# Performance work log

Hardware: AMD Instinct MI355X
Metric: run time of the kernel (lower is better)

Reference implementation:

```python
import jax, jax.numpy as jnp
import numpy as np

IN_DIM = 1024
QK_DIM = 64
NHEADS = 12
HN_MULT = 4
BATCH = 2
SEQ = 2048
BETA = 1.0 / np.sqrt(QK_DIM)


def setup_inputs() -> dict:
    key = jax.random.key(0)
    kg, kq, kk, kw = jax.random.split(key, 4)
    scale = 1.0 / np.sqrt(IN_DIM)
    g = jax.random.normal(kg, (BATCH, SEQ, IN_DIM), dtype=jnp.float32)
    Wq = jax.random.normal(kq, (NHEADS, QK_DIM, IN_DIM), dtype=jnp.float32) * scale
    Wk = jax.random.normal(kk, (NHEADS, QK_DIM, IN_DIM), dtype=jnp.float32) * scale
    Whn = jax.random.normal(kw, (HN_MULT * IN_DIM, IN_DIM), dtype=jnp.float32) * scale
    return {"g": g, "Wq": Wq, "Wk": Wk, "Whn": Whn}


def reference(g, Wq, Wk, Whn):
    # --- attention energy (Energy Transformer): E = -(1/beta) * sum logsumexp_keys(beta * q.k)
    q = jnp.einsum("bnd,hkd->bhnk", g, Wq)  # [B,H,N,K]
    k = jnp.einsum("bnd,hkd->bhnk", g, Wk)  # [B,H,N,K]
    scores = BETA * jnp.einsum("bhnk,bhmk->bhnm", q, k)  # [B,H,N(query),M(key)]
    e_attn = -(1.0 / BETA) * jnp.sum(jax.nn.logsumexp(scores, axis=-1))
    # --- Hopfield energy: -0.5 * sum(relu(W g)^2)
    h = jnp.einsum("bnd,md->bnm", g, Whn)  # [B,N,4*D]
    e_hn = -0.5 * jnp.sum(jax.nn.relu(h) ** 2)
    return e_attn + e_hn
```

## Files before the change

kernel.cpp:

```cpp
#include <hip/hip_runtime.h>
#include <hip/hip_bf16.h>

typedef __attribute__((ext_vector_type(4))) float f32x4;
typedef __attribute__((ext_vector_type(8))) short bf16x8;
typedef unsigned short u16;
typedef __attribute__((ext_vector_type(4))) u16 u16x4;


#define OFF_GB    ((size_t)0)
#define OFF_WQB   ((size_t)8388608)
#define OFF_WKB   ((size_t)(8388608+1572864))
#define OFF_WHNB  ((size_t)(8388608+2*1572864))
#define OFF_QB    (OFF_WHNB + 8388608)
#define OFF_KB    (OFF_QB + 6291456)

__device__ __forceinline__ u16 f2bf(float f) {
  union { float f; unsigned u; } x; x.f = f;
  unsigned u = x.u;
  u += 0x7fffu + ((u >> 16) & 1u);
  return (u16)(u >> 16);
}

__global__ __launch_bounds__(256) void convert_all(
    const float* __restrict__ g, const float* __restrict__ wq,
    const float* __restrict__ wk, const float* __restrict__ whn,
    u16* __restrict__ gB, u16* __restrict__ wqB, u16* __restrict__ wkB, u16* __restrict__ whnB)
{
  const int NG = 1048576;
  const int NW = 196608;
  const int total = NG + 2 * NW + NG;
  for (int i = blockIdx.x * blockDim.x + threadIdx.x; i < total; i += gridDim.x * blockDim.x) {
    const float4* src; u16* dst; int j; float scale = 1.0f;
    if (i < NG)              { src = (const float4*)g;   dst = gB;   j = i; }
    else if (i < NG + NW)    { src = (const float4*)wq;  dst = wqB;  j = i - NG; scale = 0.125f; }
    else if (i < NG + 2*NW)  { src = (const float4*)wk;  dst = wkB;  j = i - NG - NW; }
    else                     { src = (const float4*)whn; dst = whnB; j = i - NG - 2*NW; }
    float4 v = src[j];
    u16x4 o;
    o.x = f2bf(v.x * scale); o.y = f2bf(v.y * scale);
    o.z = f2bf(v.z * scale); o.w = f2bf(v.w * scale);
    *(u16x4*)(dst + (size_t)j * 4) = o;
  }
}

__global__ __launch_bounds__(256) void gemm_bt(
    const u16* __restrict__ A, const u16* __restrict__ B0, const u16* __restrict__ B1,
    u16* __restrict__ C0, u16* __restrict__ C1, int K)
{
  __shared__ u16 lA[128 * 64];
  __shared__ u16 lB[128 * 64];
  const int tid = threadIdx.x;
  const int lane = tid & 63;
  const int w = tid >> 6;
  const int bm = blockIdx.x;
  const int bn = blockIdx.y;

  const u16* Bp; u16* Cp; int bcol0;
  if (bn < 6) { Bp = B0; Cp = C0; bcol0 = bn * 128; }
  else        { Bp = B1; Cp = C1; bcol0 = (bn - 6) * 128; }
  const int arow0 = bm * 128;
  const int wr = w >> 1, wc = w & 1;
  const int l15 = lane & 15, lg = lane >> 4;

  f32x4 acc[4][4];
  const f32x4 zz = {0.f, 0.f, 0.f, 0.f};
#pragma unroll
  for (int m = 0; m < 4; m++)
#pragma unroll
    for (int n = 0; n < 4; n++) acc[m][n] = zz;

#define STAGE(KT) do {                                                                     \
    _Pragma("unroll")                                                                      \
    for (int i = 0; i < 4; i++) {                                                          \
      int rloc = w * 32 + i * 8 + (lane >> 3);                                             \
      int cb   = (((lane & 7) ^ (rloc & 7)) << 4);                                         \
      const char* srcA = (const char*)A + (((size_t)(arow0 + rloc)) * K + (KT) * 64) * 2 + cb; \
      __builtin_amdgcn_global_load_lds((const __attribute__((address_space(1))) void*)srcA, \
          (__attribute__((address_space(3))) void*)((char*)lA + (w * 32 + i * 8) * 128), 16, 0, 0); \
      const char* srcB = (const char*)Bp + (((size_t)(bcol0 + rloc)) * K + (KT) * 64) * 2 + cb; \
      __builtin_amdgcn_global_load_lds((const __attribute__((address_space(1))) void*)srcB, \
          (__attribute__((address_space(3))) void*)((char*)lB + (w * 32 + i * 8) * 128), 16, 0, 0); \
    }                                                                                      \
  } while (0)

  STAGE(0);
  const int nkt = K / 64;
  for (int kt = 0; kt < nkt; ++kt) {
    __syncthreads();
    bf16x8 a0[4], a1[4], b0[4], b1[4];
#pragma unroll
    for (int m = 0; m < 4; m++) {
      int row = wr * 64 + m * 16 + l15;
      const char* base = (const char*)lA + row * 128;
      int sw = (row & 7) << 4;
      a0[m] = *(const bf16x8*)(base + ((lg * 16) ^ sw));
      a1[m] = *(const bf16x8*)(base + ((64 + lg * 16) ^ sw));
    }
#pragma unroll
    for (int n = 0; n < 4; n++) {
      int row = wc * 64 + n * 16 + l15;
      const char* base = (const char*)lB + row * 128;
      int sw = (row & 7) << 4;
      b0[n] = *(const bf16x8*)(base + ((lg * 16) ^ sw));
      b1[n] = *(const bf16x8*)(base + ((64 + lg * 16) ^ sw));
    }
    __syncthreads();
    if (kt + 1 < nkt) STAGE(kt + 1);
#pragma unroll
    for (int m = 0; m < 4; m++)
#pragma unroll
      for (int n = 0; n < 4; n++) {
        acc[m][n] = __builtin_amdgcn_mfma_f32_16x16x32_bf16(a0[m], b0[n], acc[m][n], 0, 0, 0);
        acc[m][n] = __builtin_amdgcn_mfma_f32_16x16x32_bf16(a1[m], b1[n], acc[m][n], 0, 0, 0);
      }
  }
#pragma unroll
  for (int m = 0; m < 4; m++)
#pragma unroll
    for (int n = 0; n < 4; n++)
#pragma unroll
      for (int r = 0; r < 4; r++) {
        int row = arow0 + wr * 64 + m * 16 + lg * 4 + r;
        int col = bcol0 + wc * 64 + n * 16 + l15;
        Cp[(size_t)row * 768 + col] = f2bf(acc[m][n][r]);
      }
#undef STAGE
}

__global__ __launch_bounds__(512, 2) void hop_gemm8(
    const u16* __restrict__ A, const u16* __restrict__ Bm, float* __restrict__ out)
{
  __shared__ __align__(16) u16 lds[2][2][2][128][64];
  const int tid = threadIdx.x;
  const int lane = tid & 63, w = tid >> 6;
  const int wr = w >> 2, wc = w & 3;
  const int l15 = lane & 15, lg = lane >> 4;
  const int am0 = blockIdx.x * 256;
  const int bn0 = blockIdx.y * 256;
  constexpr int nkt = 16;

  f32x4 acc[8][4];
  const f32x4 zz = {0.f, 0.f, 0.f, 0.f};
#pragma unroll
  for (int i = 0; i < 8; i++)
#pragma unroll
    for (int j = 0; j < 4; j++) acc[i][j] = zz;

#define HSTAGE(KT, MAT, H) do {                                                            \
    const u16* s_ = (MAT) ? Bm : A;                                                        \
    int rb_ = ((MAT) ? bn0 : am0) + (H) * 128;                                             \
    char* d0_ = (char*)&lds[(KT) & 1][(MAT)][(H)][0][0];                                   \
    _Pragma("unroll")                                                                      \
    for (int q_ = 0; q_ < 2; q_++) {                                                       \
      int r_ = q_ * 64 + (tid >> 3);                                                       \
      int cb_ = ((tid & 7) * 16) ^ ((r_ & 7) << 4);                                        \
      const char* g_ = (const char*)s_ + (size_t)(rb_ + r_) * 2048 + (KT) * 128 + cb_;     \
      __builtin_amdgcn_global_load_lds((const __attribute__((address_space(1))) void*)g_,  \
          (__attribute__((address_space(3))) void*)(d0_ + q_ * 8192 + tid * 16), 16, 0, 0);\
    }                                                                                      \
  } while (0)

#define LDA_F(DST, P, I, S) do {                                                           \
    int rh_ = ((I) & 3) * 32 + wr * 16 + l15;                                              \
    const char* b_ = (const char*)&lds[(P)][0][(I) >> 2][0][0] + rh_ * 128;                \
    DST = *(const bf16x8*)(b_ + (((S) * 64 + lg * 16) ^ ((rh_ & 7) << 4)));                \
  } while (0)
#define LDB_F(DST, P, J, S) do {                                                           \
    int rh_ = ((J) & 1) * 64 + wc * 16 + l15;                                              \
    const char* b_ = (const char*)&lds[(P)][1][(J) >> 1][0][0] + rh_ * 128;                \
    DST = *(const bf16x8*)(b_ + (((S) * 64 + lg * 16) ^ ((rh_ & 7) << 4)));                \
  } while (0)

  HSTAGE(0, 0, 0); HSTAGE(0, 1, 0); HSTAGE(0, 1, 1); HSTAGE(0, 0, 1);
  HSTAGE(1, 0, 0); HSTAGE(1, 1, 0); HSTAGE(1, 1, 1);
  asm volatile("s_waitcnt vmcnt(6)" ::: "memory");
  __builtin_amdgcn_s_barrier();

  bf16x8 af[4][2], bf[4][2];

#pragma unroll 2
  for (int t = 0; t < nkt; ++t) {
    const int p = t & 1;
#pragma unroll
    for (int m = 0; m < 4; m++) { LDA_F(af[m][0], p, m, 0); LDA_F(af[m][1], p, m, 1); }
#pragma unroll
    for (int n = 0; n < 2; n++) { LDB_F(bf[n][0], p, n, 0); LDB_F(bf[n][1], p, n, 1); }
    if (t + 1 < nkt) HSTAGE(t + 1, 0, 1);
    __builtin_amdgcn_s_barrier();
    __builtin_amdgcn_s_setprio(1);
#pragma unroll
    for (int m = 0; m < 4; m++)
#pragma unroll
      for (int n = 0; n < 2; n++) {
        acc[m][n] = __builtin_amdgcn_mfma_f32_16x16x32_bf16(af[m][0], bf[n][0], acc[m][n], 0, 0, 0);
        acc[m][n] = __builtin_amdgcn_mfma_f32_16x16x32_bf16(af[m][1], bf[n][1], acc[m][n], 0, 0, 0);
      }
    __builtin_amdgcn_s_setprio(0);
    __builtin_amdgcn_s_barrier();
#pragma unroll
    for (int n = 2; n < 4; n++) { LDB_F(bf[n][0], p, n, 0); LDB_F(bf[n][1], p, n, 1); }
    if (t + 2 < nkt) HSTAGE(t + 2, 0, 0);
    __builtin_amdgcn_s_barrier();
    __builtin_amdgcn_s_setprio(1);
#pragma unroll
    for (int m = 0; m < 4; m++)
#pragma unroll
      for (int n = 2; n < 4; n++) {
        acc[m][n] = __builtin_amdgcn_mfma_f32_16x16x32_bf16(af[m][0], bf[n][0], acc[m][n], 0, 0, 0);
        acc[m][n] = __builtin_amdgcn_mfma_f32_16x16x32_bf16(af[m][1], bf[n][1], acc[m][n], 0, 0, 0);
      }
    __builtin_amdgcn_s_setprio(0);
    __builtin_amdgcn_s_barrier();
#pragma unroll
    for (int m = 0; m < 4; m++) { LDA_F(af[m][0], p, m + 4, 0); LDA_F(af[m][1], p, m + 4, 1); }
    if (t + 2 < nkt) HSTAGE(t + 2, 1, 0);
    __builtin_amdgcn_s_barrier();
    __builtin_amdgcn_s_setprio(1);
#pragma unroll
    for (int m = 0; m < 4; m++)
#pragma unroll
      for (int n = 2; n < 4; n++) {
        acc[m + 4][n] = __builtin_amdgcn_mfma_f32_16x16x32_bf16(af[m][0], bf[n][0], acc[m + 4][n], 0, 0, 0);
        acc[m + 4][n] = __builtin_amdgcn_mfma_f32_16x16x32_bf16(af[m][1], bf[n][1], acc[m + 4][n], 0, 0, 0);
      }
    __builtin_amdgcn_s_setprio(0);
    __builtin_amdgcn_s_barrier();
    if (t + 2 < nkt) HSTAGE(t + 2, 1, 1);
    __builtin_amdgcn_s_barrier();
    __builtin_amdgcn_s_setprio(1);
#pragma unroll
    for (int m = 0; m < 4; m++)
#pragma unroll
      for (int n = 0; n < 2; n++) {
        acc[m + 4][n] = __builtin_amdgcn_mfma_f32_16x16x32_bf16(af[m][0], bf[n][0], acc[m + 4][n], 0, 0, 0);
        acc[m + 4][n] = __builtin_amdgcn_mfma_f32_16x16x32_bf16(af[m][1], bf[n][1], acc[m + 4][n], 0, 0, 0);
      }
    __builtin_amdgcn_s_setprio(0);
    if (t < nkt - 2)       asm volatile("s_waitcnt vmcnt(6)" ::: "memory");
    else if (t == nkt - 2) asm volatile("s_waitcnt vmcnt(0)" ::: "memory");
    __builtin_amdgcn_s_barrier();
  }
#undef HSTAGE
#undef LDA_F
#undef LDB_F

  float loc = 0.f;
#pragma unroll
  for (int i = 0; i < 8; i++)
#pragma unroll
    for (int j = 0; j < 4; j++)
#pragma unroll
      for (int r = 0; r < 4; r++) {
        float v = acc[i][j][r];
        loc += (v > 0.f) ? v * v : 0.f;
      }
#pragma unroll
  for (int mask = 32; mask; mask >>= 1) loc += __shfl_xor(loc, mask, 64);
  if (lane == 0) atomicAdd(out, -0.5f * loc);
}

__global__ __launch_bounds__(256) void scores_lse(
    const u16* __restrict__ qB, const u16* __restrict__ kB, float* __restrict__ out)
{
  __shared__ u16 kbuf[2][128 * 64];
  const int qt = blockIdx.x;
  const int z  = blockIdx.y;
  const int b = z / 12;
  const int h = z - b * 12;
  const int tid = threadIdx.x, lane = tid & 63, w = tid >> 6;
  const int l15 = lane & 15, lg = lane >> 4;
  const size_t zb = (size_t)b * 2048;

  const size_t qrow = zb + qt * 64 + w * 16 + l15;
  const u16* qp = qB + qrow * 768 + h * 64 + lg * 8;
  bf16x8 qf0 = *(const bf16x8*)qp;
  bf16x8 qf1 = *(const bf16x8*)(qp + 32);

#define KSTAGE(KB, BUF) do {                                                               \
    _Pragma("unroll")                                                                      \
    for (int i = 0; i < 4; i++) {                                                          \
      int rloc = i * 32 + w * 8 + (lane >> 3);                                             \
      int cb   = (((lane & 7) ^ (rloc & 7)) << 4);                                         \
      const char* src = (const char*)kB + ((size_t)(zb + (KB) * 128 + rloc)) * 1536 + h * 128 + cb; \
      __builtin_amdgcn_global_load_lds((const __attribute__((address_space(1))) void*)src,  \
          (__attribute__((address_space(3))) void*)((char*)(BUF) + (i * 32 + w * 8) * 128), 16, 0, 0); \
    }                                                                                      \
  } while (0)

  f32x4 sacc = {0.f, 0.f, 0.f, 0.f};
  const f32x4 zz = {0.f, 0.f, 0.f, 0.f};

  KSTAGE(0, kbuf[0]);
  const int NKB = 16;
  for (int kb = 0; kb < NKB; ++kb) {
    __syncthreads();
    if (kb + 1 < NKB) KSTAGE(kb + 1, kbuf[(kb + 1) & 1]);
    const char* cur = (const char*)kbuf[kb & 1];
#pragma unroll
    for (int g2 = 0; g2 < 8; ++g2) {
      int row = g2 * 16 + l15;
      const char* base = cur + row * 128;
      int sw = (row & 7) << 4;
      bf16x8 b0 = *(const bf16x8*)(base + ((lg * 16) ^ sw));
      bf16x8 b1 = *(const bf16x8*)(base + ((64 + lg * 16) ^ sw));
      f32x4 s = zz;
      s = __builtin_amdgcn_mfma_f32_16x16x32_bf16(qf0, b0, s, 0, 0, 0);
      s = __builtin_amdgcn_mfma_f32_16x16x32_bf16(qf1, b1, s, 0, 0, 0);
      sacc[0] += __expf(s[0]);
      sacc[1] += __expf(s[1]);
      sacc[2] += __expf(s[2]);
      sacc[3] += __expf(s[3]);
    }
  }
#undef KSTAGE

#pragma unroll
  for (int mask = 8; mask; mask >>= 1) {
    sacc[0] += __shfl_xor(sacc[0], mask, 64);
    sacc[1] += __shfl_xor(sacc[1], mask, 64);
    sacc[2] += __shfl_xor(sacc[2], mask, 64);
    sacc[3] += __shfl_xor(sacc[3], mask, 64);
  }
  float part = 0.f;
  if (l15 == 0) {
    part = __logf(sacc[0]) + __logf(sacc[1]) + __logf(sacc[2]) + __logf(sacc[3]);
  }
  part += __shfl_xor(part, 16, 64);
  part += __shfl_xor(part, 32, 64);
  if (lane == 0) atomicAdd(out, -8.0f * part);
}

extern "C" void kernel_launch(void* const* d_in, const int* in_sizes, int n_in,
                              void* d_out, int out_size, void* d_ws, size_t ws_size,
                              hipStream_t stream)
{
  const float* g   = (const float*)d_in[0];
  const float* Wq  = (const float*)d_in[1];
  const float* Wk  = (const float*)d_in[2];
  const float* Whn = (const float*)d_in[3];
  float* out = (float*)d_out;
  char* ws = (char*)d_ws;

  u16* gB   = (u16*)(ws + OFF_GB);
  u16* wqB  = (u16*)(ws + OFF_WQB);
  u16* wkB  = (u16*)(ws + OFF_WKB);
  u16* whnB = (u16*)(ws + OFF_WHNB);
  u16* qB   = (u16*)(ws + OFF_QB);
  u16* kB   = (u16*)(ws + OFF_KB);

  hipMemsetAsync(out, 0, sizeof(float), stream);

  convert_all<<<2048, 256, 0, stream>>>(g, Wq, Wk, Whn, gB, wqB, wkB, whnB);
  gemm_bt<<<dim3(32, 12), 256, 0, stream>>>(gB, wqB, wkB, qB, kB, 1024);
  hop_gemm8<<<dim3(16, 16), 512, 0, stream>>>(gB, whnB, out);
  scores_lse<<<dim3(32, 24), 256, 0, stream>>>(qB, kB, out);
}
```

Before: 210.8 us.

## Store Q/K head-major and read K directly from global in scores kernel

The Q/K projection now writes its output in a per-(batch,head) contiguous layout [B*H][N][64] instead of row-major [B*N][768]. The scores kernel drops the LDS double-buffered K staging and its barriers and loads K fragments straight from global memory, relying on the cache, since all 32 query blocks of a head reread the same 256KB of K. Wq is pre-scaled by log2(e) so the exponent uses exp2 and the log uses the hardware log2, with the final constant adjusted (8*ln2). This trades LDS reuse and swizzling for simpler, barrier-free code that depends on L2 hit rates for K.

Result: slower. 277.3 us (+31.5%).

```diff
diff --git a/kernel.cpp b/kernel.cpp
--- a/kernel.cpp
+++ b/kernel.cpp
@@ -32,7 +32,8 @@
   for (int i = blockIdx.x * blockDim.x + threadIdx.x; i < total; i += gridDim.x * blockDim.x) {
     const float4* src; u16* dst; int j; float scale = 1.0f;
     if (i < NG)              { src = (const float4*)g;   dst = gB;   j = i; }
-    else if (i < NG + NW)    { src = (const float4*)wq;  dst = wqB;  j = i - NG; scale = 0.125f; }
+    else if (i < NG + NW)    { src = (const float4*)wq;  dst = wqB;  j = i - NG;
+                               scale = 0.125f * 1.44269504089f; }
     else if (i < NG + 2*NW)  { src = (const float4*)wk;  dst = wkB;  j = i - NG - NW; }
     else                     { src = (const float4*)whn; dst = whnB; j = i - NG - 2*NW; }
     float4 v = src[j];
@@ -122,7 +123,8 @@
       for (int r = 0; r < 4; r++) {
         int row = arow0 + wr * 64 + m * 16 + lg * 4 + r;
         int col = bcol0 + wc * 64 + n * 16 + l15;
-        Cp[(size_t)row * 768 + col] = f2bf(acc[m][n][r]);
+        size_t dst = ((((size_t)(row >> 11) * 12 + (col >> 6)) << 11) + (row & 2047)) * 64 + (col & 63);
+        Cp[dst] = f2bf(acc[m][n][r]);
       }
 #undef STAGE
 }
@@ -262,57 +264,32 @@
 __global__ __launch_bounds__(256) void scores_lse(
     const u16* __restrict__ qB, const u16* __restrict__ kB, float* __restrict__ out)
 {
-  __shared__ u16 kbuf[2][128 * 64];
   const int qt = blockIdx.x;
   const int z  = blockIdx.y;
-  const int b = z / 12;
-  const int h = z - b * 12;
   const int tid = threadIdx.x, lane = tid & 63, w = tid >> 6;
   const int l15 = lane & 15, lg = lane >> 4;
-  const size_t zb = (size_t)b * 2048;
-
-  const size_t qrow = zb + qt * 64 + w * 16 + l15;
-  const u16* qp = qB + qrow * 768 + h * 64 + lg * 8;
+
+  const u16* qp = qB + ((size_t)z * 2048 + qt * 64 + w * 16 + l15) * 64 + lg * 8;
   bf16x8 qf0 = *(const bf16x8*)qp;
   bf16x8 qf1 = *(const bf16x8*)(qp + 32);
 
-#define KSTAGE(KB, BUF) do {                                                               \
-    _Pragma("unroll")                                                                      \
-    for (int i = 0; i < 4; i++) {                                                          \
-      int rloc = i * 32 + w * 8 + (lane >> 3);                                             \
-      int cb   = (((lane & 7) ^ (rloc & 7)) << 4);                                         \
-      const char* src = (const char*)kB + ((size_t)(zb + (KB) * 128 + rloc)) * 1536 + h * 128 + cb; \
-      __builtin_amdgcn_global_load_lds((const __attribute__((address_space(1))) void*)src,  \
-          (__attribute__((address_space(3))) void*)((char*)(BUF) + (i * 32 + w * 8) * 128), 16, 0, 0); \
-    }                                                                                      \
-  } while (0)
+  const u16* kbase = kB + (size_t)z * 2048 * 64 + (size_t)l15 * 64 + lg * 8;
 
   f32x4 sacc = {0.f, 0.f, 0.f, 0.f};
   const f32x4 zz = {0.f, 0.f, 0.f, 0.f};
-
-  KSTAGE(0, kbuf[0]);
-  const int NKB = 16;
-  for (int kb = 0; kb < NKB; ++kb) {
-    __syncthreads();
-    if (kb + 1 < NKB) KSTAGE(kb + 1, kbuf[(kb + 1) & 1]);
-    const char* cur = (const char*)kbuf[kb & 1];
-#pragma unroll
-    for (int g2 = 0; g2 < 8; ++g2) {
-      int row = g2 * 16 + l15;
-      const char* base = cur + row * 128;
-      int sw = (row & 7) << 4;
-      bf16x8 b0 = *(const bf16x8*)(base + ((lg * 16) ^ sw));
-      bf16x8 b1 = *(const bf16x8*)(base + ((64 + lg * 16) ^ sw));
-      f32x4 s = zz;
-      s = __builtin_amdgcn_mfma_f32_16x16x32_bf16(qf0, b0, s, 0, 0, 0);
-      s = __builtin_amdgcn_mfma_f32_16x16x32_bf16(qf1, b1, s, 0, 0, 0);
-      sacc[0] += __expf(s[0]);
-      sacc[1] += __expf(s[1]);
-      sacc[2] += __expf(s[2]);
-      sacc[3] += __expf(s[3]);
-    }
-  }
-#undef KSTAGE
+#pragma unroll 8
+  for (int ks = 0; ks < 128; ++ks) {
+    const u16* kp = kbase + ks * 1024;
+    bf16x8 b0 = *(const bf16x8*)kp;
+    bf16x8 b1 = *(const bf16x8*)(kp + 32);
+    f32x4 s = zz;
+    s = __builtin_amdgcn_mfma_f32_16x16x32_bf16(qf0, b0, s, 0, 0, 0);
+    s = __builtin_amdgcn_mfma_f32_16x16x32_bf16(qf1, b1, s, 0, 0, 0);
+    sacc[0] += __builtin_amdgcn_exp2f(s[0]);
+    sacc[1] += __builtin_amdgcn_exp2f(s[1]);
+    sacc[2] += __builtin_amdgcn_exp2f(s[2]);
+    sacc[3] += __builtin_amdgcn_exp2f(s[3]);
+  }
 
 #pragma unroll
   for (int mask = 8; mask; mask >>= 1) {
@@ -323,11 +300,12 @@
   }
   float part = 0.f;
   if (l15 == 0) {
-    part = __logf(sacc[0]) + __logf(sacc[1]) + __logf(sacc[2]) + __logf(sacc[3]);
+    part = __builtin_amdgcn_logf(sacc[0]) + __builtin_amdgcn_logf(sacc[1]) +
+           __builtin_amdgcn_logf(sacc[2]) + __builtin_amdgcn_logf(sacc[3]);
   }
   part += __shfl_xor(part, 16, 64);
   part += __shfl_xor(part, 32, 64);
-  if (lane == 0) atomicAdd(out, -8.0f * part);
+  if (lane == 0) atomicAdd(out, -5.5451774444795625f * part);
 }
 
 extern "C" void kernel_launch(void* const* d_in, const int* in_sizes, int n_in,
@@ -348,7 +326,7 @@
   u16* qB   = (u16*)(ws + OFF_QB);
   u16* kB   = (u16*)(ws + OFF_KB);
 
-  hipMemsetAsync(out, 0, sizeof(float), stream);
+  (void)hipMemsetAsync(out, 0, sizeof(float), stream);
 
   convert_all<<<2048, 256, 0, stream>>>(g, Wq, Wk, Whn, gB, wqB, wkB, whnB);
   gemm_bt<<<dim3(32, 12), 256, 0, stream>>>(gB, wqB, wkB, qB, kB, 1024);
```
